# Performance work log

Measured on AMD Instinct MI355X. Metric: run time of the kernel, lower is better.

Reference implementation:

```python
import jax, jax.numpy as jnp
import numpy as np

D_MODEL = 1024
NUM_HEADS = 16
D_K = D_MODEL // NUM_HEADS


def setup_inputs() -> dict:
    key = jax.random.key(0)
    ks = jax.random.split(key, 11)
    s = 1.0 / np.sqrt(D_MODEL)
    return {
        "Q": jax.random.normal(ks[0], (2, 2048, D_MODEL), jnp.float32),
        "K": jax.random.normal(ks[1], (2, 2048, D_MODEL), jnp.float32),
        "V": jax.random.normal(ks[2], (2, 2048, D_MODEL), jnp.float32),
        "W_Q": jax.random.uniform(ks[3], (D_MODEL, D_MODEL), jnp.float32, -s, s),
        "b_Q": jax.random.uniform(ks[4], (D_MODEL,), jnp.float32, -s, s),
        "W_K": jax.random.uniform(ks[5], (D_K, D_MODEL), jnp.float32, -s, s),
        "b_K": jax.random.uniform(ks[6], (D_K,), jnp.float32, -s, s),
        "W_V": jax.random.uniform(ks[7], (D_K, D_MODEL), jnp.float32, -s, s),
        "b_V": jax.random.uniform(ks[8], (D_K,), jnp.float32, -s, s),
        "W_O": jax.random.uniform(ks[9], (D_MODEL, D_MODEL), jnp.float32, -s, s),
        "b_O": jax.random.uniform(ks[10], (D_MODEL,), jnp.float32, -s, s),
    }


def reference(Q, K, V, W_Q, b_Q, W_K, b_K, W_V, b_V, W_O, b_O):
    B, S, _ = Q.shape
    # Q projection -> [B, H, S, d_k]
    q = (Q @ W_Q.T + b_Q).reshape(B, S, NUM_HEADS, D_K).transpose(0, 2, 1, 3)
    # shared single-head K/V -> [B, S, d_k] (broadcast across heads)
    k = K @ W_K.T + b_K
    v = V @ W_V.T + b_V
    scale = 1.0 / jnp.sqrt(jnp.asarray(D_K, q.dtype))
    scores = jnp.einsum('bhqd,bkd->bhqk', q, k) * scale  # [B,H,S,S]
    attn = jax.nn.softmax(scores, axis=-1)
    out = jnp.einsum('bhqk,bkd->bhqd', attn, v)  # [B,H,S,d_k]
    out = out.transpose(0, 2, 1, 3).reshape(B, S, D_MODEL)
    return out @ W_O.T + b_O
```

## Files before the change

kernel.cpp:

```cpp
#include <hip/hip_runtime.h>
#include <math.h>

#define D_MODEL 1024
#define NUM_HEADS 16
#define DK 64
#define BATCH 2
#define SEQ 2048
#define MROWS (BATCH * SEQ)

typedef __attribute__((ext_vector_type(8))) short bf16x8;
typedef __attribute__((ext_vector_type(4))) short short4v;
typedef __attribute__((ext_vector_type(4))) float f32x4;

static __device__ inline short f2bf(float f) {
    union { float f; unsigned u; } v; v.f = f;
    unsigned r = v.u + 0x7FFF + ((v.u >> 16) & 1);
    return (short)(r >> 16);
}

static __device__ __forceinline__ void gload16(const void* g, void* l) {
    __builtin_amdgcn_global_load_lds(
        (const __attribute__((address_space(1))) unsigned int*)g,
        (__attribute__((address_space(3))) unsigned int*)l, 16, 0, 0);
}

__global__ __launch_bounds__(256) void cvt6(
    const float* __restrict__ q, const float* __restrict__ k,
    const float* __restrict__ v, const float* __restrict__ wq,
    const float* __restrict__ wo, const float* __restrict__ wk,
    const float* __restrict__ wv,
    short* __restrict__ qo, short* __restrict__ ko, short* __restrict__ vo,
    short* __restrict__ wqo, short* __restrict__ woo, short* __restrict__ wko,
    short* __restrict__ wvo)
{
    const int NB = (MROWS * D_MODEL) / 8;
    const int NW = (D_MODEL * D_MODEL) / 8;
    const int NS = (DK * D_MODEL) / 8;
    const int total = 3 * NB + 2 * NW + 2 * NS;
    for (int g = blockIdx.x * 256 + threadIdx.x; g < total; g += gridDim.x * 256) {
        const float* s; short* d; int x = g;
        if (x < NB)            { s = q;  d = qo;  }
        else if ((x -= NB) < NB) { s = k;  d = ko;  }
        else if ((x -= NB) < NB) { s = v;  d = vo;  }
        else if ((x -= NB) < NW) { s = wq; d = wqo; }
        else if ((x -= NW) < NW) { s = wo; d = woo; }
        else if ((x -= NW) < NS) { s = wk; d = wko; }
        else                     { x -= NS; s = wv; d = wvo; }
        float4 a = ((const float4*)s)[x * 2];
        float4 b = ((const float4*)s)[x * 2 + 1];
        bf16x8 h = {f2bf(a.x), f2bf(a.y), f2bf(a.z), f2bf(a.w),
                    f2bf(b.x), f2bf(b.y), f2bf(b.z), f2bf(b.w)};
        ((bf16x8*)d)[x] = h;
    }
}

template<int MODE, int BM, int BN>
__global__ __launch_bounds__(256) void gemm97(
    const short* __restrict__ A, const short* __restrict__ W,
    const float* __restrict__ bias, void* __restrict__ Cp,
    const short* __restrict__ A2, const short* __restrict__ W2,
    const float* __restrict__ bias2, void* __restrict__ Cp2,
    int M, int N, int K, float outmult)
{
    constexpr int MI = BM / 32;
    constexpr int NI = BN / 32;
    constexpr int ACH = BM / 32;
    constexpr int WCH = BN / 32;
    __shared__ short As[BM * 64];
    __shared__ short Ws[BN * 64];

    int sel = 0;
    if (MODE == 2) {
        sel = blockIdx.y;
        if (sel) { A = A2; W = W2; bias = bias2; Cp = Cp2; }
    }
    const int bm = blockIdx.x * BM;
    const int bn = (MODE == 2) ? 0 : blockIdx.y * BN;
    const int tid = threadIdx.x;
    const int l = tid & 63, w = tid >> 6;
    const int lr = l & 15, lg = l >> 4;
    const int wm = (w >> 1) * (BM / 2), wn = (w & 1) * (BN / 2);

    f32x4 acc[MI][NI];
    #pragma unroll
    for (int mi = 0; mi < MI; mi++)
        #pragma unroll
        for (int ni = 0; ni < NI; ni++)
            acc[mi][ni] = (f32x4){0.f, 0.f, 0.f, 0.f};

    const int srow = l >> 3;
    const int scol = (l & 7) * 8;

    for (int k0 = 0; k0 < K; k0 += 64) {
        __syncthreads();
        #pragma unroll
        for (int i = 0; i < ACH; i++) {
            int c = w * ACH + i;
            gload16(A + (size_t)(bm + 8 * c + srow) * K + k0 + scol, As + c * 512);
        }
        #pragma unroll
        for (int i = 0; i < WCH; i++) {
            int c = w * WCH + i;
            gload16(W + (size_t)(bn + 8 * c + srow) * K + k0 + scol, Ws + c * 512);
        }
        __syncthreads();
        #pragma unroll
        for (int ks = 0; ks < 2; ks++) {
            bf16x8 af[MI], bf[NI];
            #pragma unroll
            for (int mi = 0; mi < MI; mi++)
                af[mi] = *(const bf16x8*)&As[(wm + mi * 16 + lr) * 64 + ks * 32 + 8 * lg];
            #pragma unroll
            for (int ni = 0; ni < NI; ni++)
                bf[ni] = *(const bf16x8*)&Ws[(wn + ni * 16 + lr) * 64 + ks * 32 + 8 * lg];
            #pragma unroll
            for (int mi = 0; mi < MI; mi++)
                #pragma unroll
                for (int ni = 0; ni < NI; ni++)
                    acc[mi][ni] = __builtin_amdgcn_mfma_f32_16x16x32_bf16(
                        af[mi], bf[ni], acc[mi][ni], 0, 0, 0);
        }
    }

    #pragma unroll
    for (int ni = 0; ni < NI; ni++) {
        int col = bn + wn + ni * 16 + lr;
        float bv = bias[col];
        #pragma unroll
        for (int mi = 0; mi < MI; mi++) {
            #pragma unroll
            for (int r = 0; r < 4; r++) {
                int row = bm + wm + mi * 16 + lg * 4 + r;
                float val = (acc[mi][ni][r] + bv) * outmult;
                if (MODE == 0) {
                    ((short*)Cp)[(size_t)row * N + col] = f2bf(val);
                } else if (MODE == 1) {
                    ((float*)Cp)[(size_t)row * N + col] = val;
                } else {
                    if (sel == 0) {
                        ((short*)Cp)[(size_t)row * DK + col] = f2bf(val);
                    } else {
                        int bi = row >> 11, si = row & (SEQ - 1);
                        ((short*)Cp)[((size_t)bi * DK + col) * SEQ + si] = f2bf(val);
                    }
                }
            }
        }
    }
}

__global__ __launch_bounds__(256, 3) void mqa_attn_lds(
    const short* __restrict__ qb, const short* __restrict__ kb,
    const short* __restrict__ vt, short* __restrict__ ob)
{
    __shared__ char KsB[2][64 * 128];
    __shared__ char VsB[2][64 * 128];
    __shared__ char Ps[4][32 * 128];
    const int h = blockIdx.y, b = blockIdx.z;
    const int tid = threadIdx.x;
    const int l = tid & 63, w = tid >> 6;
    const int lr = l & 15, lg = l >> 4;
    const int q0 = blockIdx.x * 128 + w * 32;
    char* myPs = Ps[w];

    bf16x8 qf[2][2];
    #pragma unroll
    for (int qt = 0; qt < 2; qt++)
        #pragma unroll
        for (int kk = 0; kk < 2; kk++)
            qf[qt][kk] = *(const bf16x8*)(
                qb + (size_t)(b * SEQ + q0 + qt * 16 + lr) * D_MODEL + h * DK + kk * 32 + 8 * lg);

    int srow[2], scol[2];
    #pragma unroll
    for (int i = 0; i < 2; i++) {
        int s = i * 256 + w * 64 + l;
        srow[i] = s >> 3;
        int cb = (s & 7) * 16;
        scol[i] = (cb ^ ((srow[i] & 7) << 4)) >> 1;
    }

    f32x4 o[4][2];
    #pragma unroll
    for (int dt = 0; dt < 4; dt++)
        #pragma unroll
        for (int qt = 0; qt < 2; qt++)
            o[dt][qt] = (f32x4){0.f, 0.f, 0.f, 0.f};
    float m_i[2] = {-1e30f, -1e30f};
    float l_i[2] = {0.f, 0.f};

    #pragma unroll
    for (int i = 0; i < 2; i++) {
        gload16(kb + (size_t)(b * SEQ + 0 + srow[i]) * DK + scol[i],
                KsB[0] + (i * 256 + w * 64) * 16);
        gload16(vt + (size_t)(b * DK + srow[i]) * SEQ + 0 + scol[i],
                VsB[0] + (i * 256 + w * 64) * 16);
    }

    for (int t = 0; t < SEQ / 64; t++) {
        const int cur = t & 1;
        const int kt = t * 64;
        __syncthreads();
        if (t + 1 < SEQ / 64) {
            const int ktn = kt + 64;
            #pragma unroll
            for (int i = 0; i < 2; i++) {
                gload16(kb + (size_t)(b * SEQ + ktn + srow[i]) * DK + scol[i],
                        KsB[cur ^ 1] + (i * 256 + w * 64) * 16);
                gload16(vt + (size_t)(b * DK + srow[i]) * SEQ + ktn + scol[i],
                        VsB[cur ^ 1] + (i * 256 + w * 64) * 16);
            }
        }
        const char* Kc = KsB[cur];
        const char* Vc = VsB[cur];

        f32x4 s[2][4];
        #pragma unroll
        for (int qt = 0; qt < 2; qt++)
            #pragma unroll
            for (int j = 0; j < 4; j++) s[qt][j] = (f32x4){0.f, 0.f, 0.f, 0.f};
        #pragma unroll
        for (int kk = 0; kk < 2; kk++) {
            bf16x8 kf[4];
            #pragma unroll
            for (int j = 0; j < 4; j++) {
                int row = j * 16 + lr;
                kf[j] = *(const bf16x8*)(Kc + row * 128 + ((kk * 64 + 16 * lg) ^ ((row & 7) << 4)));
            }
            __builtin_amdgcn_s_setprio(1);
            #pragma unroll
            for (int qt = 0; qt < 2; qt++)
                #pragma unroll
                for (int j = 0; j < 4; j++)
                    s[qt][j] = __builtin_amdgcn_mfma_f32_16x16x32_bf16(
                        kf[j], qf[qt][kk], s[qt][j], 0, 0, 0);
            __builtin_amdgcn_s_setprio(0);
        }

        float corr[2];
        #pragma unroll
        for (int qt = 0; qt < 2; qt++) {
            float mx = fmaxf(fmaxf(fmaxf(s[qt][0][0], s[qt][0][1]), fmaxf(s[qt][0][2], s[qt][0][3])),
                             fmaxf(fmaxf(s[qt][1][0], s[qt][1][1]), fmaxf(s[qt][1][2], s[qt][1][3])));
            float mx2 = fmaxf(fmaxf(fmaxf(s[qt][2][0], s[qt][2][1]), fmaxf(s[qt][2][2], s[qt][2][3])),
                              fmaxf(fmaxf(s[qt][3][0], s[qt][3][1]), fmaxf(s[qt][3][2], s[qt][3][3])));
            mx = fmaxf(mx, mx2);
            mx = fmaxf(mx, __shfl_xor(mx, 16));
            mx = fmaxf(mx, __shfl_xor(mx, 32));
            float mn = fmaxf(m_i[qt], mx);
            corr[qt] = __expf(m_i[qt] - mn);
            m_i[qt] = mn;
            float rs = 0.f;
            const int row = qt * 16 + lr;
            char* base = myPs + row * 128;
            const int sw = (row & 7) << 4;
            #pragma unroll
            for (int j = 0; j < 4; j++) {
                float p0 = __expf(s[qt][j][0] - mn);
                float p1 = __expf(s[qt][j][1] - mn);
                float p2 = __expf(s[qt][j][2] - mn);
                float p3 = __expf(s[qt][j][3] - mn);
                rs += (p0 + p1) + (p2 + p3);
                short4v pk = {f2bf(p0), f2bf(p1), f2bf(p2), f2bf(p3)};
                *(short4v*)(base + ((j * 32 + lg * 8) ^ sw)) = pk;
            }
            rs += __shfl_xor(rs, 16);
            rs += __shfl_xor(rs, 32);
            l_i[qt] = l_i[qt] * corr[qt] + rs;
        }
        #pragma unroll
        for (int dt = 0; dt < 4; dt++)
            #pragma unroll
            for (int qt = 0; qt < 2; qt++)
                o[dt][qt] *= corr[qt];

        #pragma unroll
        for (int kk = 0; kk < 2; kk++) {
            bf16x8 vf[4], pf[2];
            #pragma unroll
            for (int dt = 0; dt < 4; dt++) {
                int row = dt * 16 + lr;
                vf[dt] = *(const bf16x8*)(Vc + row * 128 + ((kk * 64 + 16 * lg) ^ ((row & 7) << 4)));
            }
            #pragma unroll
            for (int qt = 0; qt < 2; qt++) {
                int row = qt * 16 + lr;
                pf[qt] = *(bf16x8*)(myPs + row * 128 + ((kk * 64 + 16 * lg) ^ ((row & 7) << 4)));
            }
            __builtin_amdgcn_s_setprio(1);
            #pragma unroll
            for (int dt = 0; dt < 4; dt++)
                #pragma unroll
                for (int qt = 0; qt < 2; qt++)
                    o[dt][qt] = __builtin_amdgcn_mfma_f32_16x16x32_bf16(
                        vf[dt], pf[qt], o[dt][qt], 0, 0, 0);
            __builtin_amdgcn_s_setprio(0);
        }
    }

    #pragma unroll
    for (int qt = 0; qt < 2; qt++) {
        float inv = 1.0f / l_i[qt];
        size_t grow = (size_t)(b * SEQ + q0 + qt * 16 + lr);
        #pragma unroll
        for (int dt = 0; dt < 4; dt++) {
            short4v pk = {f2bf(o[dt][qt][0] * inv), f2bf(o[dt][qt][1] * inv),
                          f2bf(o[dt][qt][2] * inv), f2bf(o[dt][qt][3] * inv)};
            *(short4v*)(ob + grow * D_MODEL + h * DK + dt * 16 + lg * 4) = pk;
        }
    }
}

extern "C" void kernel_launch(void* const* d_in, const int* in_sizes, int n_in,
                              void* d_out, int out_size, void* d_ws, size_t ws_size,
                              hipStream_t stream) {
    const float* Q   = (const float*)d_in[0];
    const float* K   = (const float*)d_in[1];
    const float* V   = (const float*)d_in[2];
    const float* W_Q = (const float*)d_in[3];
    const float* b_Q = (const float*)d_in[4];
    const float* W_K = (const float*)d_in[5];
    const float* b_K = (const float*)d_in[6];
    const float* W_V = (const float*)d_in[7];
    const float* b_V = (const float*)d_in[8];
    const float* W_O = (const float*)d_in[9];
    const float* b_O = (const float*)d_in[10];
    float* out = (float*)d_out;

    short* Qb  = (short*)d_ws;
    short* Kb  = Qb  + (size_t)MROWS * D_MODEL;
    short* Vb  = Kb  + (size_t)MROWS * D_MODEL;
    short* WQb = Vb  + (size_t)MROWS * D_MODEL;
    short* WKb = WQb + (size_t)D_MODEL * D_MODEL;
    short* WVb = WKb + (size_t)DK * D_MODEL;
    short* WOb = WVb + (size_t)DK * D_MODEL;
    short* qb  = WOb + (size_t)D_MODEL * D_MODEL;
    short* kb  = qb  + (size_t)MROWS * D_MODEL;
    short* vt  = kb  + (size_t)MROWS * DK;
    short* aws = vt  + (size_t)MROWS * DK;

    cvt6<<<2048, 256, 0, stream>>>(Q, K, V, W_Q, W_O, W_K, W_V,
                                   Qb, Kb, Vb, WQb, WOb, WKb, WVb);

    gemm97<0, 64, 128><<<dim3(MROWS / 64, D_MODEL / 128), 256, 0, stream>>>(
        Qb, WQb, b_Q, qb, nullptr, nullptr, nullptr, nullptr,
        MROWS, D_MODEL, D_MODEL, 0.125f);
    gemm97<2, 64, 64><<<dim3(MROWS / 64, 2), 256, 0, stream>>>(
        Kb, WKb, b_K, kb, Vb, WVb, b_V, vt, MROWS, DK, D_MODEL, 1.0f);
    mqa_attn_lds<<<dim3(SEQ / 128, NUM_HEADS, BATCH), 256, 0, stream>>>(
        qb, kb, vt, aws);
    gemm97<1, 64, 128><<<dim3(MROWS / 64, D_MODEL / 128), 256, 0, stream>>>(
        aws, WOb, b_O, out, nullptr, nullptr, nullptr, nullptr,
        MROWS, D_MODEL, D_MODEL, 1.0f);
}
```

Before: 141.3 us.

## Use exp2 softmax with folded log2e, lazy rescaling, and packed bf16 conversion

Folds log2(e) into the Q projection scale so the attention softmax can use the native exp2 instruction instead of expf. Adds a lazy online-softmax rescale that only updates the running max and rescales the accumulators when some lane's new max exceeds the old one by more than 8 (in log2 units). Replaces manual bit-twiddling bf16 rounding with the packed hardware two-float-to-bf16 conversion in the convert kernel, the P store and the output store. The lazy rescale lets unnormalized probabilities grow up to 2^8 before rescaling, which stays within fp32 range but slightly changes bf16 rounding of P.

After: 132.5 us. 1.07x faster.

```diff
diff --git a/kernel.cpp b/kernel.cpp
--- a/kernel.cpp
+++ b/kernel.cpp
@@ -1,4 +1,5 @@
 #include <hip/hip_runtime.h>
+#include <hip/hip_bf16.h>
 #include <math.h>
 
 #define D_MODEL 1024
@@ -8,14 +9,19 @@
 #define SEQ 2048
 #define MROWS (BATCH * SEQ)
 
+#define QSCALE (0.125f * 1.4426950408889634f)
+
 typedef __attribute__((ext_vector_type(8))) short bf16x8;
-typedef __attribute__((ext_vector_type(4))) short short4v;
 typedef __attribute__((ext_vector_type(4))) float f32x4;
 
-static __device__ inline short f2bf(float f) {
-    union { float f; unsigned u; } v; v.f = f;
-    unsigned r = v.u + 0x7FFF + ((v.u >> 16) & 1);
-    return (short)(r >> 16);
+static __device__ __forceinline__ short f2bf(float f) {
+    __hip_bfloat16 h = __float2bfloat16(f);
+    union { __hip_bfloat16 h; short s; } c; c.h = h; return c.s;
+}
+
+static __device__ __forceinline__ unsigned pkbf2(float a, float b) {
+    __hip_bfloat162 h = __float22bfloat162_rn(make_float2(a, b));
+    union { __hip_bfloat162 h; unsigned u; } c; c.h = h; return c.u;
 }
 
 static __device__ __forceinline__ void gload16(const void* g, void* l) {
@@ -48,9 +54,10 @@
         else                     { x -= NS; s = wv; d = wvo; }
         float4 a = ((const float4*)s)[x * 2];
         float4 b = ((const float4*)s)[x * 2 + 1];
-        bf16x8 h = {f2bf(a.x), f2bf(a.y), f2bf(a.z), f2bf(a.w),
-                    f2bf(b.x), f2bf(b.y), f2bf(b.z), f2bf(b.w)};
-        ((bf16x8*)d)[x] = h;
+        uint4 hv;
+        hv.x = pkbf2(a.x, a.y); hv.y = pkbf2(a.z, a.w);
+        hv.z = pkbf2(b.x, b.y); hv.w = pkbf2(b.z, b.w);
+        ((uint4*)d)[x] = hv;
     }
 }
 
@@ -237,42 +244,56 @@
             __builtin_amdgcn_s_setprio(0);
         }
 
-        float corr[2];
+        float corr[2]; int resc[2];
         #pragma unroll
         for (int qt = 0; qt < 2; qt++) {
-            float mx = fmaxf(fmaxf(fmaxf(s[qt][0][0], s[qt][0][1]), fmaxf(s[qt][0][2], s[qt][0][3])),
-                             fmaxf(fmaxf(s[qt][1][0], s[qt][1][1]), fmaxf(s[qt][1][2], s[qt][1][3])));
-            float mx2 = fmaxf(fmaxf(fmaxf(s[qt][2][0], s[qt][2][1]), fmaxf(s[qt][2][2], s[qt][2][3])),
-                              fmaxf(fmaxf(s[qt][3][0], s[qt][3][1]), fmaxf(s[qt][3][2], s[qt][3][3])));
-            mx = fmaxf(mx, mx2);
+            float mA = fmaxf(fmaxf(s[qt][0][0], s[qt][0][1]), s[qt][0][2]);
+            float mB = fmaxf(fmaxf(s[qt][0][3], s[qt][1][0]), s[qt][1][1]);
+            float mC = fmaxf(fmaxf(s[qt][1][2], s[qt][1][3]), s[qt][2][0]);
+            float mD = fmaxf(fmaxf(s[qt][2][1], s[qt][2][2]), s[qt][2][3]);
+            float mE = fmaxf(fmaxf(s[qt][3][0], s[qt][3][1]), s[qt][3][2]);
+            float mx = fmaxf(fmaxf(fmaxf(mA, mB), mC),
+                             fmaxf(fmaxf(mD, mE), s[qt][3][3]));
             mx = fmaxf(mx, __shfl_xor(mx, 16));
             mx = fmaxf(mx, __shfl_xor(mx, 32));
-            float mn = fmaxf(m_i[qt], mx);
-            corr[qt] = __expf(m_i[qt] - mn);
-            m_i[qt] = mn;
+
+            resc[qt] = __any(mx > m_i[qt] + 8.0f);
+            if (resc[qt]) {
+                float mn = fmaxf(m_i[qt], mx);
+                corr[qt] = __builtin_amdgcn_exp2f(m_i[qt] - mn);
+                m_i[qt] = mn;
+            } else {
+                corr[qt] = 1.0f;
+            }
+            const float mnv = m_i[qt];
+
             float rs = 0.f;
             const int row = qt * 16 + lr;
             char* base = myPs + row * 128;
             const int sw = (row & 7) << 4;
             #pragma unroll
             for (int j = 0; j < 4; j++) {
-                float p0 = __expf(s[qt][j][0] - mn);
-                float p1 = __expf(s[qt][j][1] - mn);
-                float p2 = __expf(s[qt][j][2] - mn);
-                float p3 = __expf(s[qt][j][3] - mn);
+                float p0 = __builtin_amdgcn_exp2f(s[qt][j][0] - mnv);
+                float p1 = __builtin_amdgcn_exp2f(s[qt][j][1] - mnv);
+                float p2 = __builtin_amdgcn_exp2f(s[qt][j][2] - mnv);
+                float p3 = __builtin_amdgcn_exp2f(s[qt][j][3] - mnv);
                 rs += (p0 + p1) + (p2 + p3);
-                short4v pk = {f2bf(p0), f2bf(p1), f2bf(p2), f2bf(p3)};
-                *(short4v*)(base + ((j * 32 + lg * 8) ^ sw)) = pk;
+                uint2 pk;
+                pk.x = pkbf2(p0, p1);
+                pk.y = pkbf2(p2, p3);
+                *(uint2*)(base + ((j * 32 + lg * 8) ^ sw)) = pk;
             }
             rs += __shfl_xor(rs, 16);
             rs += __shfl_xor(rs, 32);
             l_i[qt] = l_i[qt] * corr[qt] + rs;
         }
         #pragma unroll
-        for (int dt = 0; dt < 4; dt++)
-            #pragma unroll
-            for (int qt = 0; qt < 2; qt++)
-                o[dt][qt] *= corr[qt];
+        for (int qt = 0; qt < 2; qt++)
+            if (resc[qt]) {
+                #pragma unroll
+                for (int dt = 0; dt < 4; dt++)
+                    o[dt][qt] *= corr[qt];
+            }
 
         #pragma unroll
         for (int kk = 0; kk < 2; kk++) {
@@ -304,9 +325,10 @@
         size_t grow = (size_t)(b * SEQ + q0 + qt * 16 + lr);
         #pragma unroll
         for (int dt = 0; dt < 4; dt++) {
-            short4v pk = {f2bf(o[dt][qt][0] * inv), f2bf(o[dt][qt][1] * inv),
-                          f2bf(o[dt][qt][2] * inv), f2bf(o[dt][qt][3] * inv)};
-            *(short4v*)(ob + grow * D_MODEL + h * DK + dt * 16 + lg * 4) = pk;
+            uint2 pk;
+            pk.x = pkbf2(o[dt][qt][0] * inv, o[dt][qt][1] * inv);
+            pk.y = pkbf2(o[dt][qt][2] * inv, o[dt][qt][3] * inv);
+            *(uint2*)(ob + grow * D_MODEL + h * DK + dt * 16 + lg * 4) = pk;
         }
     }
 }
@@ -344,7 +366,7 @@
 
     gemm97<0, 64, 128><<<dim3(MROWS / 64, D_MODEL / 128), 256, 0, stream>>>(
         Qb, WQb, b_Q, qb, nullptr, nullptr, nullptr, nullptr,
-        MROWS, D_MODEL, D_MODEL, 0.125f);
+        MROWS, D_MODEL, D_MODEL, QSCALE);
     gemm97<2, 64, 64><<<dim3(MROWS / 64, 2), 256, 0, stream>>>(
         Kb, WKb, b_K, kb, Vb, WVb, b_V, vt, MROWS, DK, D_MODEL, 1.0f);
     mqa_attn_lds<<<dim3(SEQ / 128, NUM_HEADS, BATCH), 256, 0, stream>>>(
```
